# Kernel optimization log

Measured on AMD Instinct MI355X. Metric: run time of the kernel, lower is better.

Reference implementation:

```python
import jax, jax.numpy as jnp
import numpy as np

N = 100000   # nodes
E = 1000000  # edges
D = 128      # in_dim == out_dim (residual enabled)
EPS = 1e-5   # BatchNorm1d default eps


def setup_inputs() -> dict:
    key = jax.random.key(0)
    k = jax.random.split(key, 5)
    feature = jax.random.normal(k[0], (N, D), dtype=jnp.float32)
    src = jax.random.randint(k[1], (E,), 0, N, dtype=jnp.int32)
    dst = jax.random.randint(k[2], (E,), 0, N, dtype=jnp.int32)
    # nn.Linear(in_dim, out_dim): W is [out, in]
    W = jax.random.normal(k[3], (D, D), dtype=jnp.float32) / np.sqrt(D).astype(np.float32)
    b = jnp.zeros((D,), dtype=jnp.float32)
    gamma = jnp.ones((D,), dtype=jnp.float32)
    beta = jnp.zeros((D,), dtype=jnp.float32)
    return {"feature": feature, "src": src, "dst": dst, "W": W, "b": b,
            "gamma": gamma, "beta": beta}


def reference(feature, src, dst, W, b, gamma, beta):
    # update_all(copy_src('h'), mean): gather src features, mean-reduce onto dst
    deg = jax.ops.segment_sum(jnp.ones((E,), dtype=feature.dtype), dst,
                              num_segments=N)                      # [N]
    agg = jax.ops.segment_sum(feature[src], dst, num_segments=N)   # [N, D]
    agg = agg / jnp.maximum(deg, 1.0)[:, None]  # zero in-degree -> 0 (DGL mean)
    # NodeApplyModule: linear
    h = agg @ W.T + b                                              # [N, D]
    # BatchNorm1d over node dimension (training-mode batch stats, biased var)
    mean = jnp.mean(h, axis=0)
    var = jnp.var(h, axis=0)
    h = (h - mean) * jax.lax.rsqrt(var + EPS) * gamma + beta
    # activation, residual; dropout p=0.0 -> identity
    h = jax.nn.relu(h)
    h = feature + h
    return h
```

## Files before the change

### kernel.cpp

```cpp
#include <hip/hip_runtime.h>

typedef unsigned short u16;
typedef unsigned int u32;

#define D_DIM 128
#define CHUNK 4096
#define NSTRIPE 64
#define LCN 12800

typedef __attribute__((ext_vector_type(8))) short bf16x8;
typedef __attribute__((ext_vector_type(4))) float f32x4;

__device__ __forceinline__ float bf2f(u16 h) {
    u32 u = ((u32)h) << 16;
    return __uint_as_float(u);
}
__device__ __forceinline__ u16 f2bf(float f) {
    u32 u = __float_as_uint(f);
    u32 r = (u >> 16) & 1u;
    u += 0x7fffu + r;
    return (u16)(u >> 16);
}
__device__ __forceinline__ float lo16(u32 u) { return bf2f((u16)(u & 0xffffu)); }
__device__ __forceinline__ float hi16(u32 u) { return bf2f((u16)(u >> 16)); }

__global__ void GCNLayer_76647986365164_kernel(
        int* p, int nwords, const u32* w, int* flag,
        const float* __restrict__ f, u16* __restrict__ fb,
        const void* __restrict__ W, u16* __restrict__ wpre,
        int total8, int zb) {
    const int tid = threadIdx.x;
    const int b = blockIdx.x;
    if (b < zb) {
        int i = b * 256 + tid;
        if (i < nwords) p[i] = 0;
        return;
    }
    __shared__ int cnt;
    if (tid == 0) cnt = 0;
    __syncthreads();
    {
        int c = 0;
        for (int j = 0; j < 4; ++j) {
            u32 x = w[tid * 4 + j];
            u32 e = (x >> 7) & 0xFFu;
            if (e >= 100u && e <= 140u) c++;
        }
        atomicAdd(&cnt, c);
    }
    __syncthreads();
    const int bf = (cnt >= 700) ? 1 : 0;
    if (b == zb && tid == 0) flag[0] = bf;

    if (b == gridDim.x - 1) {
        #pragma unroll
        for (int i = 0; i < 8; ++i) {
            int idx = i * 256 + tid;
            int frag = idx >> 6, dl = idx & 63;
            int ot = frag >> 2, kt = frag & 3;
            int dg = dl >> 4, dc = dl & 15;
            int row = ot * 16 + dc, col = kt * 32 + dg * 8;
            if (bf) {
                *(uint4*)(wpre + (size_t)idx * 8) =
                    *(const uint4*)((const u16*)W + row * 128 + col);
            } else {
                const float* Wf = (const float*)W;
                float4 x = *(const float4*)(Wf + row * 128 + col);
                float4 y = *(const float4*)(Wf + row * 128 + col + 4);
                float v[8] = {x.x, x.y, x.z, x.w, y.x, y.y, y.z, y.w};
                u16 h0[8], h1[8];
                #pragma unroll
                for (int j = 0; j < 8; ++j) {
                    h0[j] = f2bf(v[j]);
                    h1[j] = f2bf(v[j] - bf2f(h0[j]));
                }
                uint4 p0, p1;
                p0.x = (u32)h0[0] | ((u32)h0[1] << 16);
                p0.y = (u32)h0[2] | ((u32)h0[3] << 16);
                p0.z = (u32)h0[4] | ((u32)h0[5] << 16);
                p0.w = (u32)h0[6] | ((u32)h0[7] << 16);
                p1.x = (u32)h1[0] | ((u32)h1[1] << 16);
                p1.y = (u32)h1[2] | ((u32)h1[3] << 16);
                p1.z = (u32)h1[4] | ((u32)h1[5] << 16);
                p1.w = (u32)h1[6] | ((u32)h1[7] << 16);
                *(uint4*)(wpre + (size_t)idx * 8) = p0;
                *(uint4*)(wpre + 16384 + (size_t)idx * 8) = p1;
            }
        }
        return;
    }
    if (bf) return;
    int i = (b - zb) * 256 + tid;
    if (i >= total8) return;
    float4 a = ((const float4*)f)[i * 2];
    float4 bb = ((const float4*)f)[i * 2 + 1];
    uint4 o;
    o.x = (u32)f2bf(a.x) | ((u32)f2bf(a.y) << 16);
    o.y = (u32)f2bf(a.z) | ((u32)f2bf(a.w) << 16);
    o.z = (u32)f2bf(bb.x) | ((u32)f2bf(bb.y) << 16);
    o.w = (u32)f2bf(bb.z) | ((u32)f2bf(bb.w) << 16);
    ((uint4*)fb)[i] = o;
}

__global__ __launch_bounds__(256)
void k_hist(const int* __restrict__ dst, int* __restrict__ cnt,
            int E, int N, int nper, int ES, int P) {
    __shared__ int lc[LCN];
    const int tid = threadIdx.x;
    const int p = blockIdx.x % P;
    const int s = blockIdx.x / P;
    const int lo = p * nper;
    const int hi = min(lo + nper, N);
    const int cn = hi - lo;
    for (int t = tid; t < cn; t += 256) lc[t] = 0;
    __syncthreads();
    const int base = s * ES;
    const int end = min(base + ES, E);
    for (int i = base + tid * 4; i < end; i += 1024) {
        if (i + 3 < end) {
            int4 d4 = *(const int4*)(dst + i);
            if (d4.x >= lo && d4.x < hi) atomicAdd(&lc[d4.x - lo], 1);
            if (d4.y >= lo && d4.y < hi) atomicAdd(&lc[d4.y - lo], 1);
            if (d4.z >= lo && d4.z < hi) atomicAdd(&lc[d4.z - lo], 1);
            if (d4.w >= lo && d4.w < hi) atomicAdd(&lc[d4.w - lo], 1);
        } else {
            for (int k = i; k < end; ++k) {
                int d = dst[k];
                if (d >= lo && d < hi) atomicAdd(&lc[d - lo], 1);
            }
        }
    }
    __syncthreads();
    int* crow = cnt + (size_t)s * N + lo;
    for (int t = tid; t < cn; t += 256) crow[t] = lc[t];
}

__global__ void k_colscan(int* __restrict__ cnt, int* __restrict__ deg, int N) {
    int n = blockIdx.x * 256 + threadIdx.x;
    if (n >= N) return;
    int run = 0;
    #pragma unroll
    for (int s = 0; s < NSTRIPE; ++s) {
        int t = cnt[(size_t)s * N + n];
        cnt[(size_t)s * N + n] = run;
        run += t;
    }
    deg[n] = run;
}

__global__ void k_scan_local(const int* deg, int* offs, int* bsums, int n) {
    __shared__ int tsum[256];
    const int tid = threadIdx.x;
    const int base = blockIdx.x * CHUNK + tid * 16;
    int v[16];
    int run = 0;
    for (int j = 0; j < 16; ++j) {
        int idx = base + j;
        v[j] = (idx < n) ? deg[idx] : 0;
        run += v[j];
    }
    tsum[tid] = run;
    __syncthreads();
    for (int off = 1; off < 256; off <<= 1) {
        int val = tsum[tid];
        int add = (tid >= off) ? tsum[tid - off] : 0;
        __syncthreads();
        tsum[tid] = val + add;
        __syncthreads();
    }
    int acc = tsum[tid] - run;
    for (int j = 0; j < 16; ++j) {
        int idx = base + j;
        if (idx < n) offs[idx] = acc;
        acc += v[j];
    }
    if (tid == 255) bsums[blockIdx.x] = tsum[255];
}

__global__ void k_scan_add(int* offs, const int* bsums, int n, int nblk) {
    __shared__ int carry_s;
    const int tid = threadIdx.x;
    const int b = blockIdx.x;
    if (tid < 64) {
        int acc = 0;
        for (int k = tid; k < b; k += 64) acc += bsums[k];
        #pragma unroll
        for (int off = 1; off < 64; off <<= 1) acc += __shfl_xor(acc, off);
        if (tid == 0) {
            carry_s = acc;
            if (b == nblk - 1) offs[n] = acc + bsums[b];
        }
    }
    __syncthreads();
    const int carry = carry_s;
    const int base = b * CHUNK + tid * 16;
    for (int j = 0; j < 16; ++j) {
        int idx = base + j;
        if (idx < n) offs[idx] += carry;
    }
}

__global__ __launch_bounds__(256)
void k_scatter(const int* __restrict__ src, const int* __restrict__ dst,
               const int* __restrict__ bases, const int* __restrict__ offs,
               int* __restrict__ csr, int E, int N, int nper, int ES, int P) {
    __shared__ int lc[LCN];
    const int tid = threadIdx.x;
    const int p = blockIdx.x % P;
    const int s = blockIdx.x / P;
    const int lo = p * nper;
    const int hi = min(lo + nper, N);
    const int cn = hi - lo;
    const int* brow = bases + (size_t)s * N;
    for (int t = tid; t < cn; t += 256)
        lc[t] = offs[lo + t] + brow[lo + t];
    __syncthreads();
    const int base = s * ES;
    const int end = min(base + ES, E);
    for (int i = base + tid * 4; i < end; i += 1024) {
        if (i + 3 < end) {
            int4 d4 = *(const int4*)(dst + i);
            int4 s4 = *(const int4*)(src + i);
            if (d4.x >= lo && d4.x < hi) csr[atomicAdd(&lc[d4.x - lo], 1)] = s4.x;
            if (d4.y >= lo && d4.y < hi) csr[atomicAdd(&lc[d4.y - lo], 1)] = s4.y;
            if (d4.z >= lo && d4.z < hi) csr[atomicAdd(&lc[d4.z - lo], 1)] = s4.z;
            if (d4.w >= lo && d4.w < hi) csr[atomicAdd(&lc[d4.w - lo], 1)] = s4.w;
        } else {
            for (int k = i; k < end; ++k) {
                int d = dst[k];
                if (d >= lo && d < hi) csr[atomicAdd(&lc[d - lo], 1)] = src[k];
            }
        }
    }
}

__global__ void k_aggregate(const void* feature, const u16* __restrict__ fcopy,
                            const int* offs, const int* csr, u16* agg,
                            const int* flag, int n, int npad) {
    const int tid = threadIdx.x;
    const int node = blockIdx.x * 16 + (tid >> 4);
    const int c = tid & 15;
    if (node >= npad) return;
    const u16* fb = flag[0] ? (const u16*)feature : fcopy;
    const uint4* fq = (const uint4*)fb;
    float acc[8];
    #pragma unroll
    for (int t = 0; t < 8; ++t) acc[t] = 0.f;
    int degn = 0;
    if (node < n) {
        int s = offs[node], e = offs[node + 1];
        degn = e - s;
        for (int j = s; j < e; j += 4) {
            int j1 = j + 1, j2 = j + 2, j3 = j + 3;
            uint4 u0 = {0,0,0,0}, u1 = {0,0,0,0}, u2 = {0,0,0,0}, u3 = {0,0,0,0};
            u0 = fq[(size_t)csr[j] * 16 + c];
            if (j1 < e) u1 = fq[(size_t)csr[j1] * 16 + c];
            if (j2 < e) u2 = fq[(size_t)csr[j2] * 16 + c];
            if (j3 < e) u3 = fq[(size_t)csr[j3] * 16 + c];
            #define ACC8(U) \
                acc[0] += lo16(U.x); acc[1] += hi16(U.x); \
                acc[2] += lo16(U.y); acc[3] += hi16(U.y); \
                acc[4] += lo16(U.z); acc[5] += hi16(U.z); \
                acc[6] += lo16(U.w); acc[7] += hi16(U.w);
            ACC8(u0); ACC8(u1); ACC8(u2); ACC8(u3);
            #undef ACC8
        }
    }
    float sc = 1.0f / (float)(degn > 1 ? degn : 1);
    uint4 o4;
    o4.x = (u32)f2bf(acc[0] * sc) | ((u32)f2bf(acc[1] * sc) << 16);
    o4.y = (u32)f2bf(acc[2] * sc) | ((u32)f2bf(acc[3] * sc) << 16);
    o4.z = (u32)f2bf(acc[4] * sc) | ((u32)f2bf(acc[5] * sc) << 16);
    o4.w = (u32)f2bf(acc[6] * sc) | ((u32)f2bf(acc[7] * sc) << 16);
    ((uint4*)(agg + (size_t)node * D_DIM))[c] = o4;
}

__global__ __launch_bounds__(512, 4)
void k_gemm(u16* __restrict__ agg, const u16* __restrict__ wpre,
            const void* __restrict__ bias, float* __restrict__ parts,
            const int* __restrict__ flag, int n) {
    __shared__ u16 sW[2048 * 8];
    const int tid = threadIdx.x;
    const int rb = blockIdx.x * 128;
    const int bf = flag[0];
    const int w = tid >> 6;
    const int lane = tid & 63;
    const int g = lane >> 4, c = lane & 15;

    bf16x8 afr[4];
    {
        const u16* arow = agg + (size_t)(rb + w * 16 + c) * D_DIM + g * 8;
        #pragma unroll
        for (int kt = 0; kt < 4; ++kt)
            afr[kt] = *(const bf16x8*)(arow + kt * 32);
    }

    f32x4 acc[8];
    #pragma unroll
    for (int ot = 0; ot < 8; ++ot) acc[ot] = (f32x4){0.f, 0.f, 0.f, 0.f};

    const int npass = bf ? 1 : 2;
    for (int pass = 0; pass < npass; ++pass) {
        if (pass) __syncthreads();
        const u16* wsrc = wpre + (size_t)pass * 16384;
        #pragma unroll
        for (int i = 0; i < 4; ++i) {
            int idx = i * 512 + tid;
            *(uint4*)(&sW[idx * 8]) = *(const uint4*)(wsrc + (size_t)idx * 8);
        }
        __syncthreads();
        #pragma unroll
        for (int ot = 0; ot < 8; ++ot) {
            #pragma unroll
            for (int kt = 0; kt < 4; ++kt) {
                bf16x8 bfr = *(const bf16x8*)(&sW[((ot * 4 + kt) * 64 + lane) * 8]);
                acc[ot] = __builtin_amdgcn_mfma_f32_16x16x32_bf16(
                    afr[kt], bfr, acc[ot], 0, 0, 0);
            }
        }
    }

    float* red = (float*)sW;
    __syncthreads();

    const int rowbase = rb + w * 16 + g * 4;
    #pragma unroll
    for (int ot = 0; ot < 8; ++ot) {
        const int o = ot * 16 + c;
        float bv = bf ? bf2f(((const u16*)bias)[o]) : ((const float*)bias)[o];
        float s = 0.f, q = 0.f;
        float hv[4];
        #pragma unroll
        for (int r = 0; r < 4; ++r) {
            float h = acc[ot][r] + bv;
            hv[r] = h;
            if (rowbase + r < n) { s += h; q += h * h; }
        }
        #pragma unroll
        for (int r = 0; r < 4; ++r) {
            float hp = __shfl_xor(hv[r], 1);
            if (!(lane & 1)) {
                u32 pk = (u32)f2bf(hv[r]) | ((u32)f2bf(hp) << 16);
                *(u32*)(agg + (size_t)(rowbase + r) * D_DIM + o) = pk;
            }
        }
        s += __shfl_xor(s, 16); s += __shfl_xor(s, 32);
        q += __shfl_xor(q, 16); q += __shfl_xor(q, 32);
        if (g == 0) { red[w * 256 + o] = s; red[w * 256 + 128 + o] = q; }
    }
    __syncthreads();
    if (tid < 256) {
        float a = 0.f;
        #pragma unroll
        for (int ww = 0; ww < 8; ++ww) a += red[ww * 256 + tid];
        parts[(size_t)blockIdx.x * 256 + tid] = a;
    }
}

__global__ void k_redstats(const float* __restrict__ partials,
                           float* __restrict__ stats, int nb) {
    const int tid = threadIdx.x;
    float a0 = 0.f, a1 = 0.f, a2 = 0.f, a3 = 0.f;
    float a4 = 0.f, a5 = 0.f, a6 = 0.f, a7 = 0.f;
    for (int r0 = blockIdx.x * 8; r0 < nb; r0 += gridDim.x * 8) {
        if (r0 + 0 < nb) a0 += partials[(size_t)(r0 + 0) * 256 + tid];
        if (r0 + 1 < nb) a1 += partials[(size_t)(r0 + 1) * 256 + tid];
        if (r0 + 2 < nb) a2 += partials[(size_t)(r0 + 2) * 256 + tid];
        if (r0 + 3 < nb) a3 += partials[(size_t)(r0 + 3) * 256 + tid];
        if (r0 + 4 < nb) a4 += partials[(size_t)(r0 + 4) * 256 + tid];
        if (r0 + 5 < nb) a5 += partials[(size_t)(r0 + 5) * 256 + tid];
        if (r0 + 6 < nb) a6 += partials[(size_t)(r0 + 6) * 256 + tid];
        if (r0 + 7 < nb) a7 += partials[(size_t)(r0 + 7) * 256 + tid];
    }
    float s = ((a0 + a1) + (a2 + a3)) + ((a4 + a5) + (a6 + a7));
    atomicAdd(&stats[tid], s);
}

__global__ void k_apply(const u16* h, const void* feature, const float* stats,
                        const void* gamma, const void* beta, void* outp,
                        const int* flag, int total8, float invn) {
    __shared__ float ssc[128], ssh[128];
    int tid = threadIdx.x;
    int bf = flag[0];
    if (tid < 128) {
        float mean = stats[tid] * invn;
        float var = stats[128 + tid] * invn - mean * mean;
        var = fmaxf(var, 0.f);
        float inv = rsqrtf(var + 1e-5f);
        float g = bf ? bf2f(((const u16*)gamma)[tid]) : ((const float*)gamma)[tid];
        float bb = bf ? bf2f(((const u16*)beta)[tid]) : ((const float*)beta)[tid];
        float sc = inv * g;
        ssc[tid] = sc;
        ssh[tid] = bb - mean * sc;
    }
    __syncthreads();
    int i = blockIdx.x * 256 + tid;
    if (i >= total8) return;
    size_t base = (size_t)i * 8;
    int c0 = (int)(base & (D_DIM - 1));
    uint4 h4 = ((const uint4*)h)[i];
    u32 hw[4] = {h4.x, h4.y, h4.z, h4.w};
    float hv[8];
    for (int j = 0; j < 4; ++j) { hv[2*j] = lo16(hw[j]); hv[2*j+1] = hi16(hw[j]); }
    float fv[8];
    if (bf) {
        uint4 f4 = ((const uint4*)feature)[i];
        u32 fw[4] = {f4.x, f4.y, f4.z, f4.w};
        for (int j = 0; j < 4; ++j) { fv[2*j] = lo16(fw[j]); fv[2*j+1] = hi16(fw[j]); }
    } else {
        float4 fa = ((const float4*)feature)[i * 2];
        float4 fb = ((const float4*)feature)[i * 2 + 1];
        fv[0]=fa.x; fv[1]=fa.y; fv[2]=fa.z; fv[3]=fa.w;
        fv[4]=fb.x; fv[5]=fb.y; fv[6]=fb.z; fv[7]=fb.w;
    }
    float ov[8];
    for (int j = 0; j < 8; ++j)
        ov[j] = fmaxf(hv[j] * ssc[c0 + j] + ssh[c0 + j], 0.f) + fv[j];
    if (bf) {
        uint4 o4;
        u32 ow[4];
        for (int j = 0; j < 4; ++j)
            ow[j] = (u32)f2bf(ov[2*j]) | ((u32)f2bf(ov[2*j+1]) << 16);
        o4.x = ow[0]; o4.y = ow[1]; o4.z = ow[2]; o4.w = ow[3];
        ((uint4*)outp)[i] = o4;
    } else {
        float4 oa, ob;
        oa.x=ov[0]; oa.y=ov[1]; oa.z=ov[2]; oa.w=ov[3];
        ob.x=ov[4]; ob.y=ov[5]; ob.z=ov[6]; ob.w=ov[7];
        ((float4*)outp)[i * 2] = oa;
        ((float4*)outp)[i * 2 + 1] = ob;
    }
}

static inline size_t al256s(size_t x) { return (x + 255) & ~(size_t)255; }
static inline int gmax1(int x) { return x > 0 ? x : 1; }
static inline size_t smax(size_t a, size_t b) { return a > b ? a : b; }

extern "C" void kernel_launch(void* const* d_in, const int* in_sizes, int n_in,
                              void* d_out, int out_size, void* d_ws, size_t ws_size,
                              hipStream_t stream) {
    const void* feature = d_in[0];
    const int*  src     = (const int*)d_in[1];
    const int*  dst     = (const int*)d_in[2];
    const void* W       = d_in[3];
    const void* bias    = d_in[4];
    const void* gamma   = d_in[5];
    const void* beta    = d_in[6];

    const int N = in_sizes[0] / D_DIM;
    const int E = in_sizes[1];
    const int Npad = (N + 127) & ~127;
    const int nblk = (N + CHUNK - 1) / CHUNK;
    const int gb   = Npad / 128;

    int P = (N + LCN - 1) / LCN;  if (P < 8) P = 8;
    const int nper = (N + P - 1) / P;
    const int ES = (((E + NSTRIPE - 1) / NSTRIPE) + 3) & ~3;

    char* p = (char*)d_ws;
    size_t o = 0;
    int*   flag   = (int*)(p + o);      o += 256;
    int*   deg    = (int*)(p + o);      o += al256s((size_t)N * 4);
    float* stats  = (float*)(p + o);    o += 256 * 4;
    o = al256s(o);
    u16*   wpre   = (u16*)(p + o);      o += al256s(2 * 16384 * 2);
    int*   bsums  = (int*)(p + o);      o += al256s(((size_t)nblk + 8) * 4);
    int*   offs   = (int*)(p + o);      o += al256s(((size_t)N + 8) * 4);
    int*   csr    = (int*)(p + o);      o += al256s((size_t)E * 4);
    float* parts  = (float*)(p + o);    o += al256s((size_t)gb * 256 * 4);
    size_t aggBytes = (size_t)Npad * D_DIM * 2;
    size_t cntBytes = (size_t)NSTRIPE * N * 4;
    u16*   agg    = (u16*)(p + o);
    int*   cnt    = (int*)(p + o);      o += al256s(smax(aggBytes, cntBytes));
    u16*   fbf    = (u16*)d_out;
    (void)ws_size; (void)n_in; (void)out_size;

    int total8 = N * D_DIM / 8;
    int zb = 1;
    int tb = gmax1((total8 + 255) / 256);
    int hblocks = NSTRIPE * P;

    GCNLayer_76647986365164_kernel<<<zb + tb + 1, 256, 0, stream>>>(
        (int*)stats, 256, (const u32*)feature, flag,
        (const float*)feature, fbf, W, wpre, total8, zb);
    k_hist<<<hblocks, 256, 0, stream>>>(dst, cnt, E, N, nper, ES, P);
    k_colscan<<<gmax1((N + 255) / 256), 256, 0, stream>>>(cnt, deg, N);
    k_scan_local<<<gmax1(nblk), 256, 0, stream>>>(deg, offs, bsums, N);
    k_scan_add<<<gmax1(nblk), 256, 0, stream>>>(offs, bsums, N, nblk);
    k_scatter<<<hblocks, 256, 0, stream>>>(src, dst, cnt, offs, csr,
                                           E, N, nper, ES, P);
    k_aggregate<<<gmax1(Npad / 16), 256, 0, stream>>>(
        feature, fbf, offs, csr, agg, flag, N, Npad);
    k_gemm<<<gmax1(gb), 512, 0, stream>>>(agg, wpre, bias, parts, flag, N);
    k_redstats<<<32, 256, 0, stream>>>(parts, stats, gb);
    k_apply<<<gmax1((total8 + 255) / 256), 256, 0, stream>>>(
        agg, feature, stats, gamma, beta, d_out, flag, total8, 1.0f / (float)N);
}
```

Measured before the change: 281.2 us.

## Fuse neighbor aggregation into GEMM kernel via shared-memory tile

Merges the mean-aggregation kernel and the linear/GEMM kernel into one. Each 512-thread block gathers and averages 128 nodes' neighbor features into an LDS tile, then runs the MFMA GEMM from that tile and reuses the same buffer for the weights. This removes the bf16 agg round trip through global memory and one kernel launch. In exchange the gather phase runs with fewer, larger blocks, each doing four passes, and the 34KB LDS tile limits occupancy, which could reduce the memory-latency hiding that the gather relies on.

```diff
diff --git a/kernel.cpp b/kernel.cpp
--- a/kernel.cpp
+++ b/kernel.cpp
@@ -234,66 +234,66 @@
     }
 }
 
-__global__ void k_aggregate(const void* feature, const u16* __restrict__ fcopy,
-                            const int* offs, const int* csr, u16* agg,
-                            const int* flag, int n, int npad) {
-    const int tid = threadIdx.x;
-    const int node = blockIdx.x * 16 + (tid >> 4);
-    const int c = tid & 15;
-    if (node >= npad) return;
-    const u16* fb = flag[0] ? (const u16*)feature : fcopy;
-    const uint4* fq = (const uint4*)fb;
-    float acc[8];
-    #pragma unroll
-    for (int t = 0; t < 8; ++t) acc[t] = 0.f;
-    int degn = 0;
-    if (node < n) {
-        int s = offs[node], e = offs[node + 1];
-        degn = e - s;
-        for (int j = s; j < e; j += 4) {
-            int j1 = j + 1, j2 = j + 2, j3 = j + 3;
-            uint4 u0 = {0,0,0,0}, u1 = {0,0,0,0}, u2 = {0,0,0,0}, u3 = {0,0,0,0};
-            u0 = fq[(size_t)csr[j] * 16 + c];
-            if (j1 < e) u1 = fq[(size_t)csr[j1] * 16 + c];
-            if (j2 < e) u2 = fq[(size_t)csr[j2] * 16 + c];
-            if (j3 < e) u3 = fq[(size_t)csr[j3] * 16 + c];
-            #define ACC8(U) \
-                acc[0] += lo16(U.x); acc[1] += hi16(U.x); \
-                acc[2] += lo16(U.y); acc[3] += hi16(U.y); \
-                acc[4] += lo16(U.z); acc[5] += hi16(U.z); \
-                acc[6] += lo16(U.w); acc[7] += hi16(U.w);
-            ACC8(u0); ACC8(u1); ACC8(u2); ACC8(u3);
-            #undef ACC8
-        }
-    }
-    float sc = 1.0f / (float)(degn > 1 ? degn : 1);
-    uint4 o4;
-    o4.x = (u32)f2bf(acc[0] * sc) | ((u32)f2bf(acc[1] * sc) << 16);
-    o4.y = (u32)f2bf(acc[2] * sc) | ((u32)f2bf(acc[3] * sc) << 16);
-    o4.z = (u32)f2bf(acc[4] * sc) | ((u32)f2bf(acc[5] * sc) << 16);
-    o4.w = (u32)f2bf(acc[6] * sc) | ((u32)f2bf(acc[7] * sc) << 16);
-    ((uint4*)(agg + (size_t)node * D_DIM))[c] = o4;
-}
-
-__global__ __launch_bounds__(512, 4)
-void k_gemm(u16* __restrict__ agg, const u16* __restrict__ wpre,
-            const void* __restrict__ bias, float* __restrict__ parts,
-            const int* __restrict__ flag, int n) {
-    __shared__ u16 sW[2048 * 8];
+__global__ __launch_bounds__(512, 8)
+void k_agg_gemm(const void* feature, const u16* __restrict__ fcopy,
+                const int* __restrict__ offs, const int* __restrict__ csr,
+                const u16* __restrict__ wpre, const void* __restrict__ bias,
+                u16* __restrict__ hout, float* __restrict__ parts,
+                const int* __restrict__ flag, int n) {
+    __shared__ u16 sBuf[128 * 136];
     const int tid = threadIdx.x;
     const int rb = blockIdx.x * 128;
     const int bf = flag[0];
+    const u16* fbp = bf ? (const u16*)feature : fcopy;
+    const uint4* fq = (const uint4*)fbp;
+
+    {
+        const int c = tid & 15;
+        for (int pass = 0; pass < 4; ++pass) {
+            const int nd = pass * 32 + (tid >> 4);
+            const int node = rb + nd;
+            float acc[8];
+            #pragma unroll
+            for (int t = 0; t < 8; ++t) acc[t] = 0.f;
+            int degn = 0;
+            if (node < n) {
+                int s = offs[node], e = offs[node + 1];
+                degn = e - s;
+                for (int j = s; j < e; j += 4) {
+                    int j1 = j + 1, j2 = j + 2, j3 = j + 3;
+                    uint4 u0 = {0,0,0,0}, u1 = {0,0,0,0};
+                    uint4 u2 = {0,0,0,0}, u3 = {0,0,0,0};
+                    u0 = fq[(size_t)csr[j] * 16 + c];
+                    if (j1 < e) u1 = fq[(size_t)csr[j1] * 16 + c];
+                    if (j2 < e) u2 = fq[(size_t)csr[j2] * 16 + c];
+                    if (j3 < e) u3 = fq[(size_t)csr[j3] * 16 + c];
+                    #define ACC8(U) \
+                        acc[0] += lo16(U.x); acc[1] += hi16(U.x); \
+                        acc[2] += lo16(U.y); acc[3] += hi16(U.y); \
+                        acc[4] += lo16(U.z); acc[5] += hi16(U.z); \
+                        acc[6] += lo16(U.w); acc[7] += hi16(U.w);
+                    ACC8(u0); ACC8(u1); ACC8(u2); ACC8(u3);
+                    #undef ACC8
+                }
+            }
+            float sc = 1.0f / (float)(degn > 1 ? degn : 1);
+            uint4 o4;
+            o4.x = (u32)f2bf(acc[0] * sc) | ((u32)f2bf(acc[1] * sc) << 16);
+            o4.y = (u32)f2bf(acc[2] * sc) | ((u32)f2bf(acc[3] * sc) << 16);
+            o4.z = (u32)f2bf(acc[4] * sc) | ((u32)f2bf(acc[5] * sc) << 16);
+            o4.w = (u32)f2bf(acc[6] * sc) | ((u32)f2bf(acc[7] * sc) << 16);
+            *(uint4*)(&sBuf[nd * 136 + c * 8]) = o4;
+        }
+    }
+    __syncthreads();
+
     const int w = tid >> 6;
     const int lane = tid & 63;
-    const int g = lane >> 4, c = lane & 15;
-
+    const int g = lane >> 4, cl = lane & 15;
     bf16x8 afr[4];
-    {
-        const u16* arow = agg + (size_t)(rb + w * 16 + c) * D_DIM + g * 8;
-        #pragma unroll
-        for (int kt = 0; kt < 4; ++kt)
-            afr[kt] = *(const bf16x8*)(arow + kt * 32);
-    }
+    #pragma unroll
+    for (int kt = 0; kt < 4; ++kt)
+        afr[kt] = *(const bf16x8*)(&sBuf[(w * 16 + cl) * 136 + g * 8 + kt * 32]);
 
     f32x4 acc[8];
     #pragma unroll
@@ -301,32 +301,32 @@
 
     const int npass = bf ? 1 : 2;
     for (int pass = 0; pass < npass; ++pass) {
-        if (pass) __syncthreads();
+        __syncthreads();
         const u16* wsrc = wpre + (size_t)pass * 16384;
         #pragma unroll
         for (int i = 0; i < 4; ++i) {
             int idx = i * 512 + tid;
-            *(uint4*)(&sW[idx * 8]) = *(const uint4*)(wsrc + (size_t)idx * 8);
+            *(uint4*)(&sBuf[idx * 8]) = *(const uint4*)(wsrc + (size_t)idx * 8);
         }
         __syncthreads();
         #pragma unroll
         for (int ot = 0; ot < 8; ++ot) {
             #pragma unroll
             for (int kt = 0; kt < 4; ++kt) {
-                bf16x8 bfr = *(const bf16x8*)(&sW[((ot * 4 + kt) * 64 + lane) * 8]);
+                bf16x8 bfr = *(const bf16x8*)(&sBuf[((ot * 4 + kt) * 64 + lane) * 8]);
                 acc[ot] = __builtin_amdgcn_mfma_f32_16x16x32_bf16(
                     afr[kt], bfr, acc[ot], 0, 0, 0);
             }
         }
     }
 
-    float* red = (float*)sW;
+    float* red = (float*)sBuf;
     __syncthreads();
 
     const int rowbase = rb + w * 16 + g * 4;
     #pragma unroll
     for (int ot = 0; ot < 8; ++ot) {
-        const int o = ot * 16 + c;
+        const int o = ot * 16 + cl;
         float bv = bf ? bf2f(((const u16*)bias)[o]) : ((const float*)bias)[o];
         float s = 0.f, q = 0.f;
         float hv[4];
@@ -341,7 +341,7 @@
             float hp = __shfl_xor(hv[r], 1);
             if (!(lane & 1)) {
                 u32 pk = (u32)f2bf(hv[r]) | ((u32)f2bf(hp) << 16);
-                *(u32*)(agg + (size_t)(rowbase + r) * D_DIM + o) = pk;
+                *(u32*)(hout + (size_t)(rowbase + r) * D_DIM + o) = pk;
             }
         }
         s += __shfl_xor(s, 16); s += __shfl_xor(s, 32);
@@ -468,10 +468,10 @@
     int*   offs   = (int*)(p + o);      o += al256s(((size_t)N + 8) * 4);
     int*   csr    = (int*)(p + o);      o += al256s((size_t)E * 4);
     float* parts  = (float*)(p + o);    o += al256s((size_t)gb * 256 * 4);
-    size_t aggBytes = (size_t)Npad * D_DIM * 2;
+    size_t hBytes   = (size_t)Npad * D_DIM * 2;
     size_t cntBytes = (size_t)NSTRIPE * N * 4;
-    u16*   agg    = (u16*)(p + o);
-    int*   cnt    = (int*)(p + o);      o += al256s(smax(aggBytes, cntBytes));
+    u16*   hbuf   = (u16*)(p + o);
+    int*   cnt    = (int*)(p + o);      o += al256s(smax(hBytes, cntBytes));
     u16*   fbf    = (u16*)d_out;
     (void)ws_size; (void)n_in; (void)out_size;
 
@@ -489,10 +489,9 @@
     k_scan_add<<<gmax1(nblk), 256, 0, stream>>>(offs, bsums, N, nblk);
     k_scatter<<<hblocks, 256, 0, stream>>>(src, dst, cnt, offs, csr,
                                            E, N, nper, ES, P);
-    k_aggregate<<<gmax1(Npad / 16), 256, 0, stream>>>(
-        feature, fbf, offs, csr, agg, flag, N, Npad);
-    k_gemm<<<gmax1(gb), 512, 0, stream>>>(agg, wpre, bias, parts, flag, N);
+    k_agg_gemm<<<gmax1(gb), 512, 0, stream>>>(
+        feature, fbf, offs, csr, wpre, bias, hbuf, parts, flag, N);
     k_redstats<<<32, 256, 0, stream>>>(parts, stats, gb);
     k_apply<<<gmax1((total8 + 255) / 256), 256, 0, stream>>>(
-        agg, feature, stats, gamma, beta, d_out, flag, total8, 1.0f / (float)N);
-}
+        hbuf, feature, stats, gamma, beta, d_out, flag, total8, 1.0f / (float)N);
+}
```

Result: faster. 270.3 us (-3.9%).
